# Kernel optimization log

Measured on AMD Instinct MI355X. Metric: run time of the kernel, lower is better.

Reference implementation:

```python
import jax, jax.numpy as jnp
import numpy as np

NUM_HEADS = 8
HEAD_DIM = 128
ATTN_SCALE = 0.12


def _rotary_tables(T, head_dim, dtype=jnp.float32):
    # modded-nanogpt half-truncated RoPE: rotate only first half of freq slots
    quarter = head_dim // 4
    angular = (1.0 / 1024.0) ** jnp.linspace(0.0, 1.0, quarter, dtype=dtype)
    angular = jnp.concatenate([angular, jnp.zeros(quarter, dtype=dtype)])  # [head_dim//2]
    t = jnp.arange(T, dtype=dtype)
    theta = t[:, None] * angular[None, :]  # [T, head_dim//2]
    return jnp.cos(theta), jnp.sin(theta)


def _apply_rotary(x, cos, sin):
    # x: [B, T, H, D]; cos/sin: [T, D//2]
    x1, x2 = jnp.split(x, 2, axis=-1)
    c = cos[None, :, None, :]
    s = sin[None, :, None, :]
    y1 = x1 * c + x2 * s
    y2 = -x1 * s + x2 * c
    return jnp.concatenate([y1, y2], axis=-1)


def _rms_norm(x):
    eps = jnp.asarray(jnp.finfo(x.dtype).eps, x.dtype)
    var = jnp.mean(jnp.square(x), axis=-1, keepdims=True)
    return x * jax.lax.rsqrt(var + eps)


def setup_inputs() -> dict:
    key = jax.random.key(0)
    k1, k2, k3, k4, k5 = jax.random.split(key, 5)
    B, T, D = 1, 4096, 1024
    hdim = NUM_HEADS * HEAD_DIM
    std = 0.5 * D ** (-0.5)
    x = jax.random.normal(k1, (B, T, D), dtype=jnp.float32)
    ve = jax.random.normal(k2, (B, T, hdim), dtype=jnp.float32)
    qkv_w = jax.random.normal(k3, (3, hdim, D), dtype=jnp.float32) * std
    lambdas = jnp.array([0.5, 0.5], dtype=jnp.float32)
    c_proj_w = jax.random.normal(k5, (D, hdim), dtype=jnp.float32) * std
    return {"x": x, "ve": ve, "qkv_w": qkv_w, "lambdas": lambdas, "c_proj_w": c_proj_w}


def reference(x, ve, qkv_w, lambdas, c_proj_w):
    B, T, D = x.shape
    H, Hd = NUM_HEADS, HEAD_DIM
    # QKV projection: qkv_w [3, H*Hd, D]
    qkv = jnp.einsum('btd,ckd->btck', x, qkv_w)  # [B, T, 3, H*Hd]
    qkv = qkv.reshape(B, T, 3, H, Hd)
    q, k, v = qkv[:, :, 0], qkv[:, :, 1], qkv[:, :, 2]  # [B, T, H, Hd]
    # QK RMSNorm
    q = _rms_norm(q)
    k = _rms_norm(k)
    # RoPE
    cos, sin = _rotary_tables(T, Hd, dtype=x.dtype)
    q = _apply_rotary(q, cos, sin)
    k = _apply_rotary(k, cos, sin)
    # value-embedding lambda mix
    v = lambdas[0] * v + lambdas[1] * ve.reshape(B, T, H, Hd)
    # causal attention with fixed scale 0.12 (block-causal FlexAttention mask)
    scores = jnp.einsum('bthd,bshd->bhts', q, k) * ATTN_SCALE  # [B, H, T, T]
    causal = jnp.tril(jnp.ones((T, T), dtype=bool))
    scores = jnp.where(causal[None, None], scores, jnp.asarray(-jnp.inf, scores.dtype))
    probs = jax.nn.softmax(scores, axis=-1)
    y = jnp.einsum('bhts,bshd->bthd', probs, v)  # [B, T, H, Hd]
    y = y.reshape(B, T, H * Hd)
    return y @ c_proj_w.T  # [B, T, D]
```

## Files before the change

### kernel.cpp

```cpp
#include <hip/hip_runtime.h>

typedef __bf16 bf16;
typedef __bf16 bf16x8 __attribute__((ext_vector_type(8)));
typedef __bf16 bf16x4 __attribute__((ext_vector_type(4)));
typedef __bf16 bf16x2 __attribute__((ext_vector_type(2)));
typedef float f32x4 __attribute__((ext_vector_type(4)));
typedef float f32x16 __attribute__((ext_vector_type(16)));
typedef int i32x4 __attribute__((ext_vector_type(4)));
typedef int i32x2 __attribute__((ext_vector_type(2)));

#define GLL16(gp, lp)                                                          \
  __builtin_amdgcn_global_load_lds(                                            \
      (const __attribute__((address_space(1))) unsigned int*)(gp),             \
      (__attribute__((address_space(3))) unsigned int*)(lp), 16, 0, 0)

__global__ __launch_bounds__(256) void cast3_f32_bf16(
    const float* __restrict__ a, bf16* __restrict__ oa, int na4,
    const float* __restrict__ b, bf16* __restrict__ ob, int nb4,
    const float* __restrict__ c, bf16* __restrict__ oc, int nc4) {
  int i = blockIdx.x * blockDim.x + threadIdx.x;
  int stride = gridDim.x * blockDim.x;
  int total = na4 + nb4 + nc4;
  for (; i < total; i += stride) {
    const float4* src;
    bf16x4* dst;
    int j = i;
    if (j < na4) {
      src = (const float4*)a + j; dst = (bf16x4*)oa + j;
    } else if ((j -= na4) < nb4) {
      src = (const float4*)b + j; dst = (bf16x4*)ob + j;
    } else {
      j -= nb4;
      src = (const float4*)c + j; dst = (bf16x4*)oc + j;
    }
    float4 v = *src;
    bf16x4 o;
    o[0] = (bf16)v.x; o[1] = (bf16)v.y; o[2] = (bf16)v.z; o[3] = (bf16)v.w;
    *dst = o;
  }
}

template <int K, int LDC, int BM, typename CT>
__global__ __launch_bounds__(256) void gemm_bt(
    const bf16* __restrict__ A, const bf16* __restrict__ B,
    CT* __restrict__ C) {
  __shared__ __align__(16) bf16 As[BM * 64];
  __shared__ __align__(16) bf16 Bs[128 * 64];
  const int tid  = threadIdx.x;
  const int lane = tid & 63;
  const int wave = tid >> 6;
  const int ln15 = lane & 15, quad = lane >> 4;
  const int wm = wave >> 1, wn = wave & 1;
  const int m0 = blockIdx.y * BM, n0 = blockIdx.x * 128;
  constexpr int MI = BM / 32;

  f32x4 acc[MI][4] = {};

  for (int k0 = 0; k0 < K; k0 += 64) {
    __syncthreads();
#pragma unroll
    for (int j = 0; j < BM / 32; ++j) {
      int gbase = j * 256 + wave * 64;
      int g = gbase + lane;
      int r = g >> 3, c = (g & 7) ^ (r & 7);
      GLL16(A + (size_t)(m0 + r) * K + k0 + c * 8, As + (size_t)gbase * 8);
    }
#pragma unroll
    for (int j = 0; j < 4; ++j) {
      int gbase = j * 256 + wave * 64;
      int g = gbase + lane;
      int r = g >> 3, c = (g & 7) ^ (r & 7);
      GLL16(B + (size_t)(n0 + r) * K + k0 + c * 8, Bs + (size_t)gbase * 8);
    }
    __syncthreads();
#pragma unroll
    for (int kk = 0; kk < 2; ++kk) {
      bf16x8 af[MI], bfr[4];
#pragma unroll
      for (int mi = 0; mi < MI; ++mi) {
        int m = wm * (BM / 2) + mi * 16 + ln15;
        int cg = kk * 4 + quad;
        af[mi] = *(const bf16x8*)(As + (m * 8 + (cg ^ (m & 7))) * 8);
      }
#pragma unroll
      for (int ni = 0; ni < 4; ++ni) {
        int n = wn * 64 + ni * 16 + ln15;
        int cg = kk * 4 + quad;
        bfr[ni] = *(const bf16x8*)(Bs + (n * 8 + (cg ^ (n & 7))) * 8);
      }
#pragma unroll
      for (int mi = 0; mi < MI; ++mi)
#pragma unroll
        for (int ni = 0; ni < 4; ++ni)
          acc[mi][ni] = __builtin_amdgcn_mfma_f32_16x16x32_bf16(
              af[mi], bfr[ni], acc[mi][ni], 0, 0, 0);
    }
  }
#pragma unroll
  for (int mi = 0; mi < MI; ++mi)
#pragma unroll
    for (int ni = 0; ni < 4; ++ni)
#pragma unroll
      for (int r = 0; r < 4; ++r) {
        int row = m0 + wm * (BM / 2) + mi * 16 + quad * 4 + r;
        int col = n0 + wn * 64 + ni * 16 + ln15;
        C[(size_t)row * LDC + col] = (CT)acc[mi][ni][r];
      }
}

__global__ __launch_bounds__(256) void qkv_post(
    const bf16* __restrict__ qkv, const float* __restrict__ ve,
    const float* __restrict__ lambdas, bf16* __restrict__ qn,
    bf16* __restrict__ kn, bf16* __restrict__ vt) {
  const int h  = blockIdx.x;
  const int t0 = blockIdx.y * 64;
  const int tid = threadIdx.x;
  const int wave = tid >> 6, lane = tid & 63;
  __shared__ __align__(16) float tile[64][129];

  const int j = lane;
  float cth = 1.0f, sth = 0.0f;
  for (int i = 0; i < 16; ++i) {
    int t = t0 + wave * 16 + i;
    if (j < 32) {
      float ang = exp2f((float)j * (-10.0f / 31.0f));
      float th = (float)t * ang;
      __sincosf(th, &sth, &cth);
    }
#pragma unroll
    for (int qk = 0; qk < 2; ++qk) {
      const bf16* row = qkv + (size_t)t * 3072 + qk * 1024 + h * 128;
      float x1 = (float)row[j], x2 = (float)row[j + 64];
      float ss = x1 * x1 + x2 * x2;
#pragma unroll
      for (int m = 1; m < 64; m <<= 1) ss += __shfl_xor(ss, m, 64);
      float rinv = rsqrtf(ss * (1.0f / 128.0f) + 1.1920929e-7f);
      if (qk == 0) rinv *= 0.12f;
      float y1 = (x1 * cth + x2 * sth) * rinv;
      float y2 = (x2 * cth - x1 * sth) * rinv;
      bf16* orow = (qk == 0 ? qn : kn) + (size_t)t * 1024 + h * 128;
      orow[j] = (bf16)y1;
      orow[j + 64] = (bf16)y2;
    }
  }

  float l0 = lambdas[0], l1 = lambdas[1];
  for (int c = 0; c < 32; ++c) {
    int idx = c * 256 + tid;
    int d = idx & 127, tl = idx >> 7;
    int t = t0 + tl;
    float v = (float)qkv[(size_t)t * 3072 + 2048 + h * 128 + d];
    float vev = ve[(size_t)t * 1024 + h * 128 + d];
    tile[tl][d] = l0 * v + l1 * vev;
  }
  __syncthreads();
  for (int c = 0; c < 32; ++c) {
    int idx = c * 256 + tid;
    int tl = idx & 63, d = idx >> 6;
    vt[((size_t)(h * 128 + d)) * 4096 + t0 + tl] = (bf16)tile[tl][d];
  }
}

__global__ __launch_bounds__(256, 2) void flash_attn(
    const bf16* __restrict__ qn, const bf16* __restrict__ kn,
    const bf16* __restrict__ vt, float* __restrict__ Op,
    float* __restrict__ ls) {
  const int id = blockIdx.x;
  const int qtile = 63 - (id >> 4);
  const int sub = id & 15;
  const int h = sub >> 1;
  const int half = sub & 1;
  const int tid = threadIdx.x;
  const int wave = tid >> 6, lane = tid & 63;
  const int l31 = lane & 31, hl = lane >> 5;
  const int qi = wave >> 1, ki = wave & 1;

  __shared__ __align__(16) bf16 smem[4 * 64 * 128];
  __shared__ float rsb[2][2][32];
  bf16* Ks = smem;
  bf16* Vs = smem + 2 * 64 * 128;

  const int q0 = qtile * 64;
  const int nkv = qtile + 1;
  const int half0 = (nkv + 1) >> 1;
  const int kt_begin = half ? half0 : 0;
  const int kt_end = half ? nkv : half0;
  const int niter = kt_end - kt_begin;
  const int pidx = (h * 64 + qtile) * 2 + half;

  if (niter == 0) {
    float4 z = {0.f, 0.f, 0.f, 0.f};
    float* opb = Op + (size_t)pidx * 8192;
#pragma unroll
    for (int j = 0; j < 8; ++j) *(float4*)(opb + tid * 32 + j * 4) = z;
    if (tid < 64) ls[pidx * 64 + tid] = 0.f;
    return;
  }

  const int qg = q0 + qi * 32 + l31;

  bf16x8 qf[8];
  {
    const bf16* qb = qn + (size_t)qg * 1024 + h * 128 + hl * 8;
#pragma unroll
    for (int f = 0; f < 8; ++f) qf[f] = *(const bf16x8*)(qb + f * 16);
  }

  f32x16 acc_o[4] = {};
  float rs = 0.0f;

  auto prefetch = [&](int kt, int buf) {
    const int kv0 = kt * 64;
    bf16* ks = Ks + buf * (64 * 128);
    bf16* vs = Vs + buf * (128 * 64);
#pragma unroll
    for (int jj = 0; jj < 4; ++jj) {
      int gbase = jj * 256 + wave * 64;
      int g = gbase + lane;
      int r = g >> 4, c = (g & 15) ^ (r & 15);
      GLL16(kn + (size_t)(kv0 + r) * 1024 + h * 128 + c * 8,
            ks + (size_t)gbase * 8);
    }
#pragma unroll
    for (int jj = 0; jj < 4; ++jj) {
      int gbase = jj * 256 + wave * 64;
      int g = gbase + lane;
      int d = g >> 3, c = (g & 7) ^ (d & 7);
      GLL16(vt + ((size_t)(h * 128 + d)) * 4096 + kv0 + c * 8,
            vs + (size_t)gbase * 8);
    }
  };

  prefetch(kt_begin, 0);

  for (int it = 0; it < niter; ++it) {
    const int kt = kt_begin + it;
    const int kv0 = kt * 64;
    __syncthreads();
    if (it + 1 < niter) prefetch(kt + 1, (it + 1) & 1);
    const bf16* ksb = Ks + (it & 1) * (64 * 128);
    const bf16* vsb = Vs + (it & 1) * (128 * 64);

    f32x16 acc0 = {}, acc1 = {};
    const int krow = ki * 32 + l31;
    __builtin_amdgcn_s_setprio(1);
#pragma unroll
    for (int f = 0; f < 4; ++f) {
      bf16x8 a0 = *(const bf16x8*)(
          ksb + (krow * 16 + ((2 * f + hl) ^ (krow & 15))) * 8);
      bf16x8 a1 = *(const bf16x8*)(
          ksb + (krow * 16 + ((2 * (f + 4) + hl) ^ (krow & 15))) * 8);
      acc0 = __builtin_amdgcn_mfma_f32_32x32x16_bf16(a0, qf[f], acc0, 0, 0, 0);
      acc1 = __builtin_amdgcn_mfma_f32_32x32x16_bf16(a1, qf[f + 4], acc1, 0, 0, 0);
    }
    __builtin_amdgcn_s_setprio(0);
    f32x16 accs = acc0 + acc1;

    const bool diag = (kt == nkv - 1);
    float pe[16];
    float rsp[4] = {0.f, 0.f, 0.f, 0.f};
    if (diag) {
#pragma unroll
      for (int r = 0; r < 16; ++r) {
        int kvl = (r & 3) + 8 * (r >> 2) + 4 * hl;
        float v = __expf(accs[r]);
        if ((kv0 + ki * 32 + kvl) > qg) v = 0.0f;
        rsp[r & 3] += v;
        pe[r] = v;
      }
    } else {
#pragma unroll
      for (int r = 0; r < 16; ++r) {
        float v = __expf(accs[r]);
        rsp[r & 3] += v;
        pe[r] = v;
      }
    }
    rs += (rsp[0] + rsp[1]) + (rsp[2] + rsp[3]);

    int pk[8];
#pragma unroll
    for (int g = 0; g < 8; ++g) {
      bf16x2 t;
      t[0] = (bf16)pe[2 * g];
      t[1] = (bf16)pe[2 * g + 1];
      pk[g] = __builtin_bit_cast(int, t);
    }

    bf16x8 pf[2];
#if __has_builtin(__builtin_amdgcn_permlane32_swap)
#pragma unroll
    for (int c = 0; c < 2; ++c) {
      i32x2 r02 = __builtin_amdgcn_permlane32_swap(pk[4 * c + 0], pk[4 * c + 2],
                                                   false, false);
      i32x2 r13 = __builtin_amdgcn_permlane32_swap(pk[4 * c + 1], pk[4 * c + 3],
                                                   false, false);
      i32x4 dv;
      dv[0] = r02[0];
      dv[1] = r13[0];
      dv[2] = r02[1];
      dv[3] = r13[1];
      pf[c] = __builtin_bit_cast(bf16x8, dv);
    }
#else
#pragma unroll
    for (int c = 0; c < 2; ++c) {
      int sh0 = __shfl_xor(pk[4 * c + 0], 32, 64);
      int sh1 = __shfl_xor(pk[4 * c + 1], 32, 64);
      int sh2 = __shfl_xor(pk[4 * c + 2], 32, 64);
      int sh3 = __shfl_xor(pk[4 * c + 3], 32, 64);
      int own0 = hl ? pk[4 * c + 2] : pk[4 * c + 0];
      int own1 = hl ? pk[4 * c + 3] : pk[4 * c + 1];
      int par0 = hl ? sh2 : sh0;
      int par1 = hl ? sh3 : sh1;
      i32x4 dv;
      dv[0] = hl ? par0 : own0;
      dv[1] = hl ? par1 : own1;
      dv[2] = hl ? own0 : par0;
      dv[3] = hl ? own1 : par1;
      pf[c] = __builtin_bit_cast(bf16x8, dv);
    }
#endif

    __builtin_amdgcn_s_setprio(1);
#pragma unroll
    for (int dt = 0; dt < 4; ++dt) {
      int vrow = dt * 32 + l31;
#pragma unroll
      for (int c = 0; c < 2; ++c) {
        bf16x8 a = *(const bf16x8*)(
            vsb + (vrow * 8 + ((4 * ki + 2 * c + hl) ^ (vrow & 7))) * 8);
        acc_o[dt] =
            __builtin_amdgcn_mfma_f32_32x32x16_bf16(a, pf[c], acc_o[dt], 0, 0, 0);
      }
    }
    __builtin_amdgcn_s_setprio(0);
  }

  rs += __shfl_xor(rs, 32, 64);
  __syncthreads();
  if (lane < 32) rsb[qi][ki][l31] = rs;
  float* ob = (float*)smem;
  if (ki == 1) {
#pragma unroll
    for (int dt = 0; dt < 4; ++dt)
#pragma unroll
      for (int r = 0; r < 16; ++r) {
        int d = dt * 32 + (r & 3) + 8 * (r >> 2) + 4 * hl;
        ob[(qi * 32 + l31) * 129 + d] = acc_o[dt][r];
      }
  }
  __syncthreads();
  if (ki == 0) {
    float lsum = rsb[qi][0][l31] + rsb[qi][1][l31];
    if (hl == 0) ls[pidx * 64 + qi * 32 + l31] = lsum;
    float* opb = Op + (size_t)pidx * 8192 + (qi * 32 + l31) * 128;
#pragma unroll
    for (int dt = 0; dt < 4; ++dt)
#pragma unroll
      for (int rg = 0; rg < 4; ++rg) {
        float4 o;
        int d0 = dt * 32 + 4 * hl + 8 * rg;
        o.x = acc_o[dt][rg * 4 + 0] + ob[(qi * 32 + l31) * 129 + d0 + 0];
        o.y = acc_o[dt][rg * 4 + 1] + ob[(qi * 32 + l31) * 129 + d0 + 1];
        o.z = acc_o[dt][rg * 4 + 2] + ob[(qi * 32 + l31) * 129 + d0 + 2];
        o.w = acc_o[dt][rg * 4 + 3] + ob[(qi * 32 + l31) * 129 + d0 + 3];
        *(float4*)(opb + d0) = o;
      }
  }
}

__global__ __launch_bounds__(256) void attn_combine(
    const float* __restrict__ Op, const float* __restrict__ ls,
    bf16* __restrict__ y) {
  int gid = blockIdx.x * 256 + threadIdx.x;
  int t = gid >> 8;
  int c4 = gid & 255;
  int qtile = t >> 6, ql = t & 63;
  int h = c4 >> 5;
  int d = (c4 & 31) * 4;
  int pbase = (h * 64 + qtile) * 2;
  const float4 o0 = *(const float4*)(Op + (size_t)pbase * 8192 + ql * 128 + d);
  const float4 o1 =
      *(const float4*)(Op + (size_t)(pbase + 1) * 8192 + ql * 128 + d);
  float inv = 1.0f / (ls[pbase * 64 + ql] + ls[(pbase + 1) * 64 + ql]);
  bf16x4 o;
  o[0] = (bf16)((o0.x + o1.x) * inv);
  o[1] = (bf16)((o0.y + o1.y) * inv);
  o[2] = (bf16)((o0.z + o1.z) * inv);
  o[3] = (bf16)((o0.w + o1.w) * inv);
  *(bf16x4*)(y + (size_t)t * 1024 + h * 128 + d) = o;
}

extern "C" void kernel_launch(void* const* d_in, const int* in_sizes, int n_in,
                              void* d_out, int out_size, void* d_ws,
                              size_t ws_size, hipStream_t stream) {
  const float* x       = (const float*)d_in[0];
  const float* ve      = (const float*)d_in[1];
  const float* qkv_w   = (const float*)d_in[2];
  const float* lambdas = (const float*)d_in[3];
  const float* c_proj  = (const float*)d_in[4];
  float* out = (float*)d_out;

  char* ws = (char*)d_ws;
  bf16* qkv   = (bf16*)ws;
  bf16* xbf   = (bf16*)(ws + 25165824);
  bf16* wqkv  = (bf16*)(ws + 33554432);
  bf16* wproj = (bf16*)(ws + 39845888);
  bf16* qn    = (bf16*)(ws + 41943040);
  bf16* kn    = (bf16*)(ws + 50331648);
  bf16* vt    = (bf16*)(ws + 58720256);
  bf16* yb    = (bf16*)(ws + 67108864);
  float* Op  = (float*)ws;
  float* lsw = (float*)(ws + 33554432);

  cast3_f32_bf16<<<2048, 256, 0, stream>>>(x, xbf, 4194304 / 4, qkv_w, wqkv,
                                           3145728 / 4, c_proj, wproj,
                                           1048576 / 4);

  gemm_bt<1024, 3072, 128, bf16><<<dim3(24, 32), 256, 0, stream>>>(xbf, wqkv,
                                                                   qkv);

  qkv_post<<<dim3(8, 64), 256, 0, stream>>>(qkv, ve, lambdas, qn, kn, vt);

  flash_attn<<<1024, 256, 0, stream>>>(qn, kn, vt, Op, lsw);
  attn_combine<<<4096, 256, 0, stream>>>(Op, lsw, yb);

  gemm_bt<1024, 1024, 64, float><<<dim3(8, 64), 256, 0, stream>>>(yb, wproj,
                                                                  out);
}
```

Measured before the change: 227.1 us.

## Use 128-row query tiles with per-wave full-KV processing in flash attention

```diff
diff --git a/kernel.cpp b/kernel.cpp
--- a/kernel.cpp
+++ b/kernel.cpp
@@ -166,38 +166,27 @@
     const bf16* __restrict__ vt, float* __restrict__ Op,
     float* __restrict__ ls) {
   const int id = blockIdx.x;
-  const int qtile = 63 - (id >> 4);
+  const int qt = (id < 256) ? (31 - (id >> 4)) : ((id - 256) >> 4);
   const int sub = id & 15;
   const int h = sub >> 1;
   const int half = sub & 1;
   const int tid = threadIdx.x;
   const int wave = tid >> 6, lane = tid & 63;
   const int l31 = lane & 31, hl = lane >> 5;
-  const int qi = wave >> 1, ki = wave & 1;
 
   __shared__ __align__(16) bf16 smem[4 * 64 * 128];
-  __shared__ float rsb[2][2][32];
   bf16* Ks = smem;
   bf16* Vs = smem + 2 * 64 * 128;
 
-  const int q0 = qtile * 64;
-  const int nkv = qtile + 1;
-  const int half0 = (nkv + 1) >> 1;
+  const int nkv = 2 * (qt + 1);
+  const int half0 = qt + 1;
   const int kt_begin = half ? half0 : 0;
   const int kt_end = half ? nkv : half0;
   const int niter = kt_end - kt_begin;
-  const int pidx = (h * 64 + qtile) * 2 + half;
-
-  if (niter == 0) {
-    float4 z = {0.f, 0.f, 0.f, 0.f};
-    float* opb = Op + (size_t)pidx * 8192;
-#pragma unroll
-    for (int j = 0; j < 8; ++j) *(float4*)(opb + tid * 32 + j * 4) = z;
-    if (tid < 64) ls[pidx * 64 + tid] = 0.f;
-    return;
-  }
-
-  const int qg = q0 + qi * 32 + l31;
+  const int pidx = (h * 32 + qt) * 2 + half;
+
+  const int qminw = qt * 128 + wave * 32;
+  const int qg = qminw + l31;
 
   bf16x8 qf[8];
   {
@@ -241,76 +230,86 @@
     const bf16* ksb = Ks + (it & 1) * (64 * 128);
     const bf16* vsb = Vs + (it & 1) * (128 * 64);
 
+    if (kv0 > qminw + 31) continue;
+
     f32x16 acc0 = {}, acc1 = {};
-    const int krow = ki * 32 + l31;
+    const int l15 = l31 & 15;
     __builtin_amdgcn_s_setprio(1);
 #pragma unroll
-    for (int f = 0; f < 4; ++f) {
+    for (int f = 0; f < 8; ++f) {
       bf16x8 a0 = *(const bf16x8*)(
-          ksb + (krow * 16 + ((2 * f + hl) ^ (krow & 15))) * 8);
+          ksb + (l31 * 16 + ((2 * f + hl) ^ l15)) * 8);
       bf16x8 a1 = *(const bf16x8*)(
-          ksb + (krow * 16 + ((2 * (f + 4) + hl) ^ (krow & 15))) * 8);
+          ksb + ((32 + l31) * 16 + ((2 * f + hl) ^ l15)) * 8);
       acc0 = __builtin_amdgcn_mfma_f32_32x32x16_bf16(a0, qf[f], acc0, 0, 0, 0);
-      acc1 = __builtin_amdgcn_mfma_f32_32x32x16_bf16(a1, qf[f + 4], acc1, 0, 0, 0);
+      acc1 = __builtin_amdgcn_mfma_f32_32x32x16_bf16(a1, qf[f], acc1, 0, 0, 0);
     }
     __builtin_amdgcn_s_setprio(0);
-    f32x16 accs = acc0 + acc1;
-
-    const bool diag = (kt == nkv - 1);
-    float pe[16];
+
+    const bool needmask = (kv0 + 63 > qminw);
     float rsp[4] = {0.f, 0.f, 0.f, 0.f};
-    if (diag) {
+    if (needmask) {
 #pragma unroll
       for (int r = 0; r < 16; ++r) {
         int kvl = (r & 3) + 8 * (r >> 2) + 4 * hl;
-        float v = __expf(accs[r]);
-        if ((kv0 + ki * 32 + kvl) > qg) v = 0.0f;
-        rsp[r & 3] += v;
-        pe[r] = v;
+        float v0 = __expf(acc0[r]);
+        float v1 = __expf(acc1[r]);
+        if (kv0 + kvl > qg) v0 = 0.0f;
+        if (kv0 + 32 + kvl > qg) v1 = 0.0f;
+        acc0[r] = v0; acc1[r] = v1;
+        rsp[r & 3] += v0 + v1;
       }
     } else {
 #pragma unroll
       for (int r = 0; r < 16; ++r) {
-        float v = __expf(accs[r]);
-        rsp[r & 3] += v;
-        pe[r] = v;
+        float v0 = __expf(acc0[r]);
+        float v1 = __expf(acc1[r]);
+        acc0[r] = v0; acc1[r] = v1;
+        rsp[r & 3] += v0 + v1;
       }
     }
     rs += (rsp[0] + rsp[1]) + (rsp[2] + rsp[3]);
 
-    int pk[8];
+    int pk0[8], pk1[8];
 #pragma unroll
     for (int g = 0; g < 8; ++g) {
-      bf16x2 t;
-      t[0] = (bf16)pe[2 * g];
-      t[1] = (bf16)pe[2 * g + 1];
-      pk[g] = __builtin_bit_cast(int, t);
-    }
-
-    bf16x8 pf[2];
+      bf16x2 t0, t1;
+      t0[0] = (bf16)acc0[2 * g]; t0[1] = (bf16)acc0[2 * g + 1];
+      t1[0] = (bf16)acc1[2 * g]; t1[1] = (bf16)acc1[2 * g + 1];
+      pk0[g] = __builtin_bit_cast(int, t0);
+      pk1[g] = __builtin_bit_cast(int, t1);
+    }
+
+    bf16x8 pf[4];
 #if __has_builtin(__builtin_amdgcn_permlane32_swap)
 #pragma unroll
-    for (int c = 0; c < 2; ++c) {
-      i32x2 r02 = __builtin_amdgcn_permlane32_swap(pk[4 * c + 0], pk[4 * c + 2],
-                                                   false, false);
-      i32x2 r13 = __builtin_amdgcn_permlane32_swap(pk[4 * c + 1], pk[4 * c + 3],
-                                                   false, false);
+    for (int cc = 0; cc < 4; ++cc) {
+      int s0 = (cc < 2) ? pk0[(cc & 1) * 4 + 0] : pk1[(cc & 1) * 4 + 0];
+      int s1 = (cc < 2) ? pk0[(cc & 1) * 4 + 1] : pk1[(cc & 1) * 4 + 1];
+      int s2 = (cc < 2) ? pk0[(cc & 1) * 4 + 2] : pk1[(cc & 1) * 4 + 2];
+      int s3 = (cc < 2) ? pk0[(cc & 1) * 4 + 3] : pk1[(cc & 1) * 4 + 3];
+      i32x2 r02 = __builtin_amdgcn_permlane32_swap(s0, s2, false, false);
+      i32x2 r13 = __builtin_amdgcn_permlane32_swap(s1, s3, false, false);
       i32x4 dv;
       dv[0] = r02[0];
       dv[1] = r13[0];
       dv[2] = r02[1];
       dv[3] = r13[1];
-      pf[c] = __builtin_bit_cast(bf16x8, dv);
+      pf[cc] = __builtin_bit_cast(bf16x8, dv);
     }
 #else
 #pragma unroll
-    for (int c = 0; c < 2; ++c) {
-      int sh0 = __shfl_xor(pk[4 * c + 0], 32, 64);
-      int sh1 = __shfl_xor(pk[4 * c + 1], 32, 64);
-      int sh2 = __shfl_xor(pk[4 * c + 2], 32, 64);
-      int sh3 = __shfl_xor(pk[4 * c + 3], 32, 64);
-      int own0 = hl ? pk[4 * c + 2] : pk[4 * c + 0];
-      int own1 = hl ? pk[4 * c + 3] : pk[4 * c + 1];
+    for (int cc = 0; cc < 4; ++cc) {
+      int s0 = (cc < 2) ? pk0[(cc & 1) * 4 + 0] : pk1[(cc & 1) * 4 + 0];
+      int s1 = (cc < 2) ? pk0[(cc & 1) * 4 + 1] : pk1[(cc & 1) * 4 + 1];
+      int s2 = (cc < 2) ? pk0[(cc & 1) * 4 + 2] : pk1[(cc & 1) * 4 + 2];
+      int s3 = (cc < 2) ? pk0[(cc & 1) * 4 + 3] : pk1[(cc & 1) * 4 + 3];
+      int sh0 = __shfl_xor(s0, 32, 64);
+      int sh1 = __shfl_xor(s1, 32, 64);
+      int sh2 = __shfl_xor(s2, 32, 64);
+      int sh3 = __shfl_xor(s3, 32, 64);
+      int own0 = hl ? s2 : s0;
+      int own1 = hl ? s3 : s1;
       int par0 = hl ? sh2 : sh0;
       int par1 = hl ? sh3 : sh1;
       i32x4 dv;
@@ -318,7 +317,7 @@
       dv[1] = hl ? par1 : own1;
       dv[2] = hl ? own0 : par0;
       dv[3] = hl ? own1 : par1;
-      pf[c] = __builtin_bit_cast(bf16x8, dv);
+      pf[cc] = __builtin_bit_cast(bf16x8, dv);
     }
 #endif
 
@@ -327,47 +326,31 @@
     for (int dt = 0; dt < 4; ++dt) {
       int vrow = dt * 32 + l31;
 #pragma unroll
-      for (int c = 0; c < 2; ++c) {
+      for (int cc = 0; cc < 4; ++cc) {
         bf16x8 a = *(const bf16x8*)(
-            vsb + (vrow * 8 + ((4 * ki + 2 * c + hl) ^ (vrow & 7))) * 8);
+            vsb + (vrow * 8 + ((2 * cc + hl) ^ (vrow & 7))) * 8);
         acc_o[dt] =
-            __builtin_amdgcn_mfma_f32_32x32x16_bf16(a, pf[c], acc_o[dt], 0, 0, 0);
+            __builtin_amdgcn_mfma_f32_32x32x16_bf16(a, pf[cc], acc_o[dt], 0, 0, 0);
       }
     }
     __builtin_amdgcn_s_setprio(0);
   }
 
   rs += __shfl_xor(rs, 32, 64);
-  __syncthreads();
-  if (lane < 32) rsb[qi][ki][l31] = rs;
-  float* ob = (float*)smem;
-  if (ki == 1) {
-#pragma unroll
-    for (int dt = 0; dt < 4; ++dt)
-#pragma unroll
-      for (int r = 0; r < 16; ++r) {
-        int d = dt * 32 + (r & 3) + 8 * (r >> 2) + 4 * hl;
-        ob[(qi * 32 + l31) * 129 + d] = acc_o[dt][r];
-      }
-  }
-  __syncthreads();
-  if (ki == 0) {
-    float lsum = rsb[qi][0][l31] + rsb[qi][1][l31];
-    if (hl == 0) ls[pidx * 64 + qi * 32 + l31] = lsum;
-    float* opb = Op + (size_t)pidx * 8192 + (qi * 32 + l31) * 128;
-#pragma unroll
-    for (int dt = 0; dt < 4; ++dt)
-#pragma unroll
-      for (int rg = 0; rg < 4; ++rg) {
-        float4 o;
-        int d0 = dt * 32 + 4 * hl + 8 * rg;
-        o.x = acc_o[dt][rg * 4 + 0] + ob[(qi * 32 + l31) * 129 + d0 + 0];
-        o.y = acc_o[dt][rg * 4 + 1] + ob[(qi * 32 + l31) * 129 + d0 + 1];
-        o.z = acc_o[dt][rg * 4 + 2] + ob[(qi * 32 + l31) * 129 + d0 + 2];
-        o.w = acc_o[dt][rg * 4 + 3] + ob[(qi * 32 + l31) * 129 + d0 + 3];
-        *(float4*)(opb + d0) = o;
-      }
-  }
+  if (hl == 0) ls[pidx * 128 + wave * 32 + l31] = rs;
+  float* opb = Op + (size_t)pidx * 16384 + (size_t)(wave * 32 + l31) * 128;
+#pragma unroll
+  for (int dt = 0; dt < 4; ++dt)
+#pragma unroll
+    for (int rg = 0; rg < 4; ++rg) {
+      float4 o;
+      o.x = acc_o[dt][rg * 4 + 0];
+      o.y = acc_o[dt][rg * 4 + 1];
+      o.z = acc_o[dt][rg * 4 + 2];
+      o.w = acc_o[dt][rg * 4 + 3];
+      int d0 = dt * 32 + 4 * hl + 8 * rg;
+      *(float4*)(opb + d0) = o;
+    }
 }
 
 __global__ __launch_bounds__(256) void attn_combine(
@@ -376,14 +359,14 @@
   int gid = blockIdx.x * 256 + threadIdx.x;
   int t = gid >> 8;
   int c4 = gid & 255;
-  int qtile = t >> 6, ql = t & 63;
+  int qt = t >> 7, ql = t & 127;
   int h = c4 >> 5;
   int d = (c4 & 31) * 4;
-  int pbase = (h * 64 + qtile) * 2;
-  const float4 o0 = *(const float4*)(Op + (size_t)pbase * 8192 + ql * 128 + d);
+  int pb = (h * 32 + qt) * 2;
+  const float4 o0 = *(const float4*)(Op + (size_t)pb * 16384 + ql * 128 + d);
   const float4 o1 =
-      *(const float4*)(Op + (size_t)(pbase + 1) * 8192 + ql * 128 + d);
-  float inv = 1.0f / (ls[pbase * 64 + ql] + ls[(pbase + 1) * 64 + ql]);
+      *(const float4*)(Op + (size_t)(pb + 1) * 16384 + ql * 128 + d);
+  float inv = 1.0f / (ls[pb * 128 + ql] + ls[(pb + 1) * 128 + ql]);
   bf16x4 o;
   o[0] = (bf16)((o0.x + o1.x) * inv);
   o[1] = (bf16)((o0.y + o1.y) * inv);
@@ -423,7 +406,7 @@
 
   qkv_post<<<dim3(8, 64), 256, 0, stream>>>(qkv, ve, lambdas, qn, kn, vt);
 
-  flash_attn<<<1024, 256, 0, stream>>>(qn, kn, vt, Op, lsw);
+  flash_attn<<<512, 256, 0, stream>>>(qn, kn, vt, Op, lsw);
   attn_combine<<<4096, 256, 0, stream>>>(Op, lsw, yb);
 
   gemm_bt<1024, 1024, 64, float><<<dim3(8, 64), 256, 0, stream>>>(yb, wproj,
```

New measurement: 224.3 us. About the same (-1.2%).
